# Optimization experiments

Hardware: AMD Instinct MI355X
Metric: run time of the kernel (lower is better)

Reference implementation:

```python
import jax, jax.numpy as jnp
import numpy as np

B, F, C, W_, H_ = 4, 8, 256, 7, 7   # batch, frames, compressed channels (in_dim//r), width, height
CIN = 2048                          # in_dim
CH = CIN // 16                      # in_dim // (2*r) = 128, per-branch q/k channels


def _pw2d(x, W, b):
    # 1x1 Conv2d == per-pixel channel matmul. x: (N,Cin,H,W), W: (Cout,Cin)
    return jnp.einsum('nchw,oc->nohw', x, W) + b[None, :, None, None]


def setup_inputs() -> dict:
    key = jax.random.key(0)
    ks = iter(jax.random.split(key, 40))
    def rn(shape, s=0.02):
        return jax.random.normal(next(ks), shape, dtype=jnp.float32) * s
    inp = {
        'x':       rn((B * F, CIN, H_, W_), 1.0),
        'domainX': rn((B * F, CIN, H_, W_), 1.0),
        'domainY': rn((B * F, 1, H_, W_), 1.0),
        # conv1_1_pre (1 -> 2048), output is discarded in forward but computed faithfully
        'w_pre': rn((CIN, 1)), 'b_pre': rn((CIN,)),
        # conv3 (2048 -> 256); its weight is SHARED with layer1_downconv and layer1_downconv_Y
        'w_conv3': rn((C, CIN)), 'b_conv3': rn((C,)),
        # value_conv 1x1x1 Conv3d (256 -> 2048); weight SHARED with layer1_upconv(_Y)
        'w_value': rn((CIN, C)), 'b_value': rn((CIN,)),
        # tied-weight convs have their own biases
        'b_l1down': rn((C,)), 'b_l1up': rn((CIN,)),
        'b_l1down_Y': rn((C,)), 'b_l1up_Y': rn((CIN,)),
        # layer2 convs: independent weights (layer2_*gamma init to 0, so init add is a no-op)
        'w_l2down': rn((C, CIN)), 'b_l2down': rn((C,)),
        'w_l2up': rn((CIN, C)), 'b_l2up': rn((CIN,)),
        'w_l2down_Y': rn((C, CIN)), 'b_l2down_Y': rn((C,)),
        'w_l2up_Y': rn((CIN, C)), 'b_l2up_Y': rn((CIN,)),
        # q/k projections (2048 -> 128 each)
        'w_c11': rn((CH, CIN)), 'b_c11': rn((CH,)),
        'w_c12': rn((CH, CIN)), 'b_c12': rn((CH,)),
        'w_c21': rn((CH, CIN)), 'b_c21': rn((CH,)),
        'w_c22': rn((CH, CIN)), 'b_c22': rn((CH,)),
        'pos_embedV': rn((1, F, C * H_ * W_), 1.0),
        'gamma': jnp.asarray(0.01, dtype=jnp.float32),
    }
    return inp


def reference(x, domainX, domainY, w_pre, b_pre, w_conv3, b_conv3, w_value, b_value,
              b_l1down, b_l1up, b_l1down_Y, b_l1up_Y,
              w_l2down, b_l2down, w_l2up, b_l2up,
              w_l2down_Y, b_l2down_Y, w_l2up_Y, b_l2up_Y,
              w_c11, b_c11, w_c12, b_c12, w_c21, b_c21, w_c22, b_c22,
              pos_embedV, gamma):
    S = F * W_ * H_  # 392 tokens per clip
    # conv1_1_pre output is overwritten in the original forward (dead computation)
    _dead = _pw2d(domainY, w_pre, b_pre)
    del _dead
    # domainY path: down(conv3 weight) -> up(value_conv weight) -> layer2 down -> layer2 up
    # (create5D/create4D + permutes + 1x1x1 conv3d collapse to pointwise channel matmuls)
    dY = _pw2d(_pw2d(_pw2d(_pw2d(domainX, w_conv3, b_l1down_Y), w_value, b_l1up_Y),
                     w_l2down_Y, b_l2down_Y), w_l2up_Y, b_l2up_Y)
    q4 = jnp.concatenate([_pw2d(x, w_c11, b_c11), _pw2d(dY, w_c12, b_c12)], axis=1)  # (32,256,7,7)
    q = q4.reshape(B, F, C, W_, H_).transpose(0, 1, 3, 4, 2).reshape(B, S, C)
    # domainX path (same structure, shared layer1 weights, its own biases)
    dX = _pw2d(_pw2d(_pw2d(_pw2d(domainX, w_conv3, b_l1down), w_value, b_l1up),
                     w_l2down, b_l2down), w_l2up, b_l2up)
    k4 = jnp.concatenate([_pw2d(x, w_c21, b_c21), _pw2d(dX, w_c22, b_c22)], axis=1)
    k5 = k4.reshape(B, F, C, W_, H_).transpose(0, 1, 3, 4, 2)        # (B,F,W,H,C)
    k = k5.transpose(0, 2, 1, 3, 4).reshape(B, C, S)                 # faithful odd permute
    # value: conv3 -> +pos_embed -> rearrange to (B, S, C)
    v4 = _pw2d(x, w_conv3, b_conv3)                                  # (32,256,7,7)
    v = v4.reshape(B, F, C * W_ * H_) + pos_embedV                   # dropout p=0 is identity
    v = v.reshape(B, F, C, W_, H_).transpose(0, 1, 3, 4, 2).reshape(B, S, C)
    attn = jax.nn.softmax(jnp.einsum('bnc,bcm->bnm', q, k), axis=-1)  # (B,392,392)
    out = jnp.einsum('bnm,bmc->bnc', attn, v)
    out = out.reshape(B, F, W_, H_, C).transpose(0, 4, 1, 2, 3)      # (B,C,F,W,H)
    out = jnp.einsum('bcthw,oc->bothw', out, w_value) + b_value[None, :, None, None, None]
    out = out.transpose(0, 2, 1, 3, 4).reshape(B * F, CIN, W_, H_)
    return (gamma * out + x) * out + x
```

## Files before the change

kernel.cpp:

```cpp
#include <hip/hip_runtime.h>
#include <hip/hip_bf16.h>


typedef __attribute__((ext_vector_type(8))) _Float16 half8;
typedef __attribute__((ext_vector_type(4))) float f32x4;

#define TOKENS 1568

__device__ __forceinline__ ushort f2h(float f) {
    _Float16 h = (_Float16)f;
    return *(ushort*)&h;
}
__device__ __forceinline__ float h2f(ushort u) {
    _Float16 h = *(_Float16*)&u;
    return (float)h;
}

__device__ __forceinline__ void gl16(const void* g, void* l) {
    __builtin_amdgcn_global_load_lds(
        (const __attribute__((address_space(1))) unsigned int*)g,
        (__attribute__((address_space(3))) unsigned int*)l, 16, 0, 0);
}

#define EPI_PART  0
#define EPI_F16   1
#define EPI_FINAL 2

struct GA {
    const ushort* Ah; int lda; long sA;
    const ushort* Wh; int ldw; long sW;
    const float* bias; int sB;
    int nkc, Kc;
    float* fO; ushort* bO;
    int ldc; long sC; int M, N;
    int nx, ny;
    const float *ex, *gamma; float* fout;
};

template<int EPI>
__device__ __forceinline__ void gmm_body(const GA g, int bx, int by, int bzf,
                                         ushort* LA, ushort* LW)
{
    const int tid = threadIdx.x;
    const int bz = bzf / g.nkc;
    const int kc = bzf % g.nkc;
    const int row0 = by * 64, col0 = bx * 128;

    const int srow = tid >> 2;
    const int sq   = (tid & 3) ^ (srow & 3);
    int am  = row0 + srow;      if (am  > g.M - 1) am  = g.M - 1;
    int wn0 = col0 + srow;      if (wn0 > g.N - 1) wn0 = g.N - 1;
    int wn1 = col0 + 64 + srow; if (wn1 > g.N - 1) wn1 = g.N - 1;
    const long kbase = (long)kc * g.Kc + sq * 8;
    const ushort* gA  = g.Ah + bz * g.sA + (long)am  * g.lda + kbase;
    const ushort* gW0 = g.Wh + bz * g.sW + (long)wn0 * g.ldw + kbase;
    const ushort* gW1 = g.Wh + bz * g.sW + (long)wn1 * g.ldw + kbase;
    const int wb = (tid & 192) * 8;

    auto STAGE = [&](int buf, int k0) {
        gl16(gA + k0, LA + buf * 2048 + wb);
        gl16(gW0 + k0, LW + buf * 4096 + wb);
        gl16(gW1 + k0, LW + buf * 4096 + 2048 + wb);
    };

    const int lane = tid & 63, wv = tid >> 6;
    const int wr = (wv >> 1) * 32, wc = (wv & 1) * 64;
    const int fr = lane & 15;
    const int ksw = ((lane >> 4) ^ (lane & 3)) * 8;
    int aoff[2], boff[4];
#pragma unroll
    for (int mi = 0; mi < 2; ++mi) aoff[mi] = (wr + mi * 16 + fr) * 32 + ksw;
#pragma unroll
    for (int ni = 0; ni < 4; ++ni) boff[ni] = (wc + ni * 16 + fr) * 32 + ksw;

    f32x4 acc[2][4];
#pragma unroll
    for (int mi = 0; mi < 2; ++mi)
#pragma unroll
        for (int ni = 0; ni < 4; ++ni) acc[mi][ni] = (f32x4){0.f, 0.f, 0.f, 0.f};

    STAGE(0, 0);
    __syncthreads();
    int cur = 0;
    for (int k0 = 0; k0 < g.Kc; k0 += 32) {
        if (k0 + 32 < g.Kc) STAGE(cur ^ 1, k0 + 32);

        half8 fa[2], fb[4];
#pragma unroll
        for (int mi = 0; mi < 2; ++mi) fa[mi] = *(half8*)&LA[cur * 2048 + aoff[mi]];
#pragma unroll
        for (int ni = 0; ni < 4; ++ni) fb[ni] = *(half8*)&LW[cur * 4096 + boff[ni]];
#pragma unroll
        for (int mi = 0; mi < 2; ++mi)
#pragma unroll
            for (int ni = 0; ni < 4; ++ni)
                acc[mi][ni] = __builtin_amdgcn_mfma_f32_16x16x32_f16(fa[mi], fb[ni], acc[mi][ni], 0, 0, 0);
        __syncthreads();
        cur ^= 1;
    }

    const int q4 = (lane >> 4) * 4;
    float gg = 0.f;
    if constexpr (EPI == EPI_FINAL) gg = g.gamma[0];
#pragma unroll
    for (int mi = 0; mi < 2; ++mi)
#pragma unroll
        for (int ni = 0; ni < 4; ++ni)
#pragma unroll
            for (int qi = 0; qi < 4; ++qi) {
                int m = row0 + wr + mi * 16 + q4 + qi;
                int n = col0 + wc + ni * 16 + fr;
                if (m >= g.M || n >= g.N) continue;
                float v = acc[mi][ni][qi];
                if (g.bias) v += g.bias[bz * g.sB + n];
                if constexpr (EPI == EPI_PART) {
                    g.fO[(long)bzf * g.sC + (long)m * g.ldc + n] = v;
                } else if constexpr (EPI == EPI_F16) {
                    g.bO[(long)bzf * g.sC + (long)m * g.ldc + n] = f2h(v);
                } else {
                    int nimg = m / 49, p = m % 49;
                    long xi = (long)nimg * (2048 * 49) + (long)n * 49 + p;
                    float xv = g.ex[xi];
                    g.fout[xi] = (gg * v + xv) * v + xv;
                }
            }
}

template<int EPI>
__global__ __launch_bounds__(256)
void gmm(GA g)
{
    __shared__ __align__(16) ushort LA[2 * 2048], LW[2 * 4096];
    gmm_body<EPI>(g, blockIdx.x, blockIdx.y, blockIdx.z, LA, LW);
}

__global__ __launch_bounds__(256)
void gmm3(GA g1, int n1, GA g2, int n2, GA g3)
{
    __shared__ __align__(16) ushort LA[2 * 2048], LW[2 * 4096];
    int id = blockIdx.x;
    if (id < n1) {
        int bx = id % g1.nx, t = id / g1.nx;
        gmm_body<EPI_PART>(g1, bx, t % g1.ny, t / g1.ny, LA, LW);
    } else if (id < n1 + n2) {
        id -= n1;
        int bx = id % g2.nx, t = id / g2.nx;
        gmm_body<EPI_PART>(g2, bx, t % g2.ny, t / g2.ny, LA, LW);
    } else {
        id -= n1 + n2;
        int bx = id % g3.nx, t = id / g3.nx;
        gmm_body<EPI_PART>(g3, bx, t % g3.ny, t / g3.ny, LA, LW);
    }
}

__global__ __launch_bounds__(256)
void prep(const float* c11, const float* c21, const float* conv3,
          const float* c22, const float* c12, const float* wval,
          const float* w2dX, const float* w2dY,
          const float* b_c11, const float* b_c21, const float* b_conv3,
          const float* x, const float* dX,
          const float* w2u, const float* w2uY, const float* wv, const float* w3,
          ushort* Wg1, ushort* C2, ushort* Wval, ushort* W2dS, float* bg1,
          ushort* Xt, ushort* DXt,
          ushort* W2uT, ushort* WvT, ushort* W3T)
{
    __shared__ float tile[64][65];
    int b = blockIdx.x;
    int tid = threadIdx.x;
    if (b < 12290) {
        int e = b * 256 + tid;
        if (e < 1048576) {
            float v = e < 262144 ? c11[e] : e < 524288 ? c21[e - 262144] : conv3[e - 524288];
            Wg1[e] = f2h(v);
        } else if (e < 1572864) {
            int i = e - 1048576;
            C2[i] = f2h(i < 262144 ? c22[i] : c12[i - 262144]);
        } else if (e < 2097152) {
            int i = e - 1572864; Wval[i] = f2h(wval[i]);
        } else if (e < 2097664) {
            int i = e - 2097152;
            bg1[i] = i < 128 ? b_c11[i] : i < 256 ? b_c21[i - 128] : b_conv3[i - 256];
        } else {
            int i = e - 2097664;
            W2dS[i] = f2h(i < 524288 ? w2dX[i] : w2dY[i - 524288]);
        }
    } else if (b < 14338) {
        int local = b - 12290;
        int z = local >> 10;
        int rem = local & 1023;
        int n = rem & 31, c0 = (rem >> 5) * 64;
        const float* src = z ? dX : x;
        ushort* oh = z ? DXt : Xt;
        const float* s = src + (long)n * (2048 * 49) + (long)c0 * 49;
        for (int idx = tid; idx < 64 * 49; idx += 256)
            tile[idx / 49][idx % 49] = s[idx];
        __syncthreads();
        for (int idx = tid; idx < 49 * 64; idx += 256) {
            int p = idx >> 6, cl = idx & 63;
            long o = (long)(n * 49 + p) * 2048 + c0 + cl;
            oh[o] = f2h(tile[cl][p]);
        }
    } else {
        int local = b - 14338;
        int zc = local >> 7, t = local & 127;
        const float* src; ushort* dh; int rows;
        switch (zc) {
            case 0:  src = w2u;  dh = W2uT;          rows = 2048; break;
            case 1:  src = w2uY; dh = W2uT + 524288; rows = 2048; break;
            case 2:  src = wv;   dh = WvT;           rows = 2048; break;
            default: src = w3;   dh = W3T;           rows = 256;  break;
        }
        int cols = 524288 / rows;
        int tilesX = cols >> 6;
        int tx = t % tilesX, ty = t / tilesX;
        for (int i = tid; i < 4096; i += 256) {
            int r = i >> 6, c = i & 63;
            tile[r][c] = src[(long)(ty * 64 + r) * cols + tx * 64 + c];
        }
        __syncthreads();
        for (int i = tid; i < 4096; i += 256) {
            int c = i >> 6, r = i & 63;
            long o = (long)(tx * 64 + c) * rows + ty * 64 + r;
            dh[o] = f2h(tile[r][c]);
        }
    }
}

__global__ __launch_bounds__(256)
void redA(const float* __restrict__ PG1, const float* __restrict__ bg1,
          const float* __restrict__ pos,
          ushort* Q, ushort* Km, ushort* V,
          const float* __restrict__ A1p, ushort* A1,
          const float* __restrict__ Dp, ushort* DT,
          const float* w2dX, const float* w2dY,
          const float* b1dX, const float* b1uX, const float* b2dX,
          const float* b1dY, const float* b1uY, const float* b2dY,
          float* __restrict__ dvec)
{
    int blk = blockIdx.x, tid = threadIdx.x;
    if (blk < 3136) {
        int idx = blk * 256 + tid;
        int m = idx >> 9, n = idx & 511;
        float v = bg1[n];
#pragma unroll
        for (int k = 0; k < 8; ++k) v += PG1[(long)k * 802816 + idx];
        int p = m % 49, img = m / 49;
        int f = img & 7, b = img >> 3;
        if (n < 128) {
            Q[m * 256 + n] = f2h(v);
        } else if (n < 256) {
            int c = n - 128;
            int flat = (p / 7) * 14336 + f * 1792 + (p % 7) * 256 + c;
            int ci = flat / 392, mm = flat % 392;
            Km[(long)b * 100352 + (long)mm * 256 + ci] = f2h(v);
        } else {
            int c = n - 256;
            v += pos[f * 12544 + c * 49 + p];
            int s = m % 392;
            long o = (long)b * 106496 + (long)c * 416 + s;
            V[o] = f2h(v);
            if (s < 24) V[o + 392] = 0;
        }
    } else if (blk < 3200) {
        int b2 = blk - 3136;
#pragma unroll
        for (int r = 0; r < 4; ++r) {
            int idx = b2 * 1024 + r * 256 + tid;
            int z = idx >> 15, e = idx & 32767;
            float v = 0.f;
#pragma unroll
            for (int k = 0; k < 8; ++k) v += A1p[(long)(z * 8 + k) * 32768 + e];
            A1[idx] = f2h(v);
        }
    } else if (blk < 3232) {
        int b2 = blk - 3200;
#pragma unroll
        for (int r = 0; r < 16; ++r) {
            int idx = b2 * 4096 + r * 256 + tid;
            int z = idx >> 16, e = idx & 65535;
            int i = e >> 8, j = e & 255;
            float v = 0.f;
#pragma unroll
            for (int k = 0; k < 8; ++k) v += Dp[(long)(z * 8 + k) * 65536 + e];
            DT[(long)z * 65536 + (long)j * 256 + i] = f2h(v);
        }
    } else {
        int blk2 = blk - 3232;
        int z = blk2 >> 6;
        int lane = tid & 63, wv = tid >> 6;
        int c = (blk2 & 63) * 4 + wv;
        const float* w2d = (z ? w2dY : w2dX) + (long)c * 2048;
        const float* b1d = z ? b1dY : b1dX;
        const float* b1u = z ? b1uY : b1uX;
        const float* b2d = z ? b2dY : b2dX;
        float acc = 0.f;
        for (int o = lane; o < 2048; o += 64) acc = fmaf(w2d[o], b1u[o], acc);
        for (int j = lane; j < 256; j += 64) {
            float d = 0.f;
#pragma unroll
            for (int k = 0; k < 8; ++k) d += Dp[(long)(z * 8 + k) * 65536 + (long)c * 256 + j];
            acc = fmaf(d, b1d[j], acc);
        }
        for (int off = 32; off; off >>= 1) acc += __shfl_down(acc, off, 64);
        if (lane == 0) dvec[z * 256 + c] = acc + b2d[c];
    }
}

__global__ __launch_bounds__(256)
void mkc(GA gM,
         const ushort* __restrict__ A1, const float* __restrict__ dvec,
         const float* c22, const float* c12,
         const float* b2uX, const float* b2uY,
         const float* bc22, const float* bc12, float* kc)
{
    __shared__ __align__(16) ushort LA[2 * 2048], LW[2 * 4096];
    int id = blockIdx.x;
    if (id < 64) {
        gmm_body<EPI_F16>(gM, id & 15, (id >> 4) & 1, id >> 5, LA, LW);
        return;
    }
    int tid = threadIdx.x, lane = tid & 63, wv = tid >> 6;
    int w = (id - 64) * 4 + wv;
    int z = w >> 7, i = w & 127;
    const ushort* a1 = A1 + (long)z * 32768 + i * 256;
    const float* dv = dvec + z * 256;
    const float* cr = (z ? c12 : c22) + (long)i * 2048;
    const float* b2u = z ? b2uY : b2uX;
    float acc = 0.f;
    for (int c = lane; c < 256; c += 64) acc = fmaf(h2f(a1[c]), dv[c], acc);
    for (int o = lane; o < 2048; o += 64) acc = fmaf(cr[o], b2u[o], acc);
    for (int off = 32; off; off >>= 1) acc += __shfl_down(acc, off, 64);
    if (lane == 0) kc[z * 128 + i] = acc + (z ? bc12 : bc22)[i];
}

__global__ __launch_bounds__(256)
void r_qk2(const float* __restrict__ P, const float* __restrict__ kc,
           ushort* Q, ushort* Km)
{
    int idx = blockIdx.x * 256 + threadIdx.x;
    int m = idx >> 8, j = idx & 255;
    float v = kc[j];
#pragma unroll
    for (int k = 0; k < 8; ++k) v += P[(long)k * 401408 + idx];
    ushort h = f2h(v);
    if (j < 128) {
        int c = 128 + j;
        int p = m % 49, img = m / 49, f = img & 7, b = img >> 3;
        int flat = (p / 7) * 14336 + f * 1792 + (p % 7) * 256 + c;
        int ci = flat / 392, mm = flat % 392;
        Km[(long)b * 100352 + (long)mm * 256 + ci] = h;
    } else {
        Q[m * 256 + j] = h;
    }
}

__global__ __launch_bounds__(256)
void fattn(const ushort* __restrict__ Qg, const ushort* __restrict__ Kmg,
           const ushort* __restrict__ VT, ushort* __restrict__ O)
{
    __shared__ float raw[16 * 420];
    __shared__ ushort P[16 * 424];
    const int b = blockIdx.y;
    const int r0 = blockIdx.x * 16;
    const int tid = threadIdx.x;
    const int lane = tid & 63, wv = tid >> 6;
    const int fr = lane & 15, g = lane >> 4;
    const int kb = g * 8;
    const long base = (long)b * 100352;
    const long vbase = (long)b * 106496;

    int qr = r0 + fr; if (qr > 391) qr = 391;
    const ushort* qp = Qg + base + (long)qr * 256 + kb;
    half8 qh[8];
#pragma unroll
    for (int kf = 0; kf < 8; ++kf) qh[kf] = *(const half8*)(qp + kf * 32);

    for (int nf = wv; nf < 26; nf += 4) {
        int kcol = nf * 16 + fr; if (kcol > 391) kcol = 391;
        const ushort* kp = Kmg + base + (long)kcol * 256 + kb;
        f32x4 a = (f32x4){0.f, 0.f, 0.f, 0.f};
#pragma unroll
        for (int kf = 0; kf < 8; ++kf) {
            half8 bh = *(const half8*)(kp + kf * 32);
            a = __builtin_amdgcn_mfma_f32_16x16x32_f16(qh[kf], bh, a, 0, 0, 0);
        }
#pragma unroll
        for (int q = 0; q < 4; ++q)
            raw[(g * 4 + q) * 420 + nf * 16 + fr] = a[q];
    }
    __syncthreads();

    {
        int row = tid >> 4, j = tid & 15;
        float v[26];
        float m = -1e30f;
#pragma unroll
        for (int k = 0; k < 26; ++k) {
            int col = j + 16 * k;
            v[k] = (col < 392) ? raw[row * 420 + col] : -1e30f;
            m = fmaxf(m, v[k]);
        }
#pragma unroll
        for (int off = 8; off; off >>= 1) m = fmaxf(m, __shfl_xor(m, off, 16));
        float s = 0.f;
#pragma unroll
        for (int k = 0; k < 26; ++k) { v[k] = __expf(v[k] - m); s += v[k]; }
#pragma unroll
        for (int off = 8; off; off >>= 1) s += __shfl_xor(s, off, 16);
        float inv = 1.f / s;
#pragma unroll
        for (int k = 0; k < 26; ++k) {
            int col = j + 16 * k;
            P[row * 424 + col] = (col < 392) ? f2h(v[k] * inv) : (ushort)0;
        }
    }
    __syncthreads();

    const int cf0 = wv * 4;
    f32x4 o[4];
#pragma unroll
    for (int c = 0; c < 4; ++c) o[c] = (f32x4){0.f, 0.f, 0.f, 0.f};
#pragma unroll
    for (int kf = 0; kf < 13; ++kf) {
        half8 pa = *(half8*)&P[fr * 424 + kf * 32 + kb];
#pragma unroll
        for (int c = 0; c < 4; ++c) {
            const ushort* vp = VT + vbase + (long)((cf0 + c) * 16 + fr) * 416 + kf * 32 + kb;
            half8 vb = *(const half8*)vp;
            o[c] = __builtin_amdgcn_mfma_f32_16x16x32_f16(pa, vb, o[c], 0, 0, 0);
        }
    }
#pragma unroll
    for (int c = 0; c < 4; ++c)
#pragma unroll
        for (int q = 0; q < 4; ++q) {
            int orow = r0 + g * 4 + q;
            if (orow < 392)
                O[base + (long)orow * 256 + (cf0 + c) * 16 + fr] = f2h(o[c][q]);
        }
}

extern "C" void kernel_launch(void* const* d_in, const int* in_sizes, int n_in,
                              void* d_out, int out_size, void* d_ws, size_t ws_size,
                              hipStream_t stream)
{
    const float* x        = (const float*)d_in[0];
    const float* domainX  = (const float*)d_in[1];
    const float* w_conv3  = (const float*)d_in[5];
    const float* b_conv3  = (const float*)d_in[6];
    const float* w_value  = (const float*)d_in[7];
    const float* b_value  = (const float*)d_in[8];
    const float* b_l1down   = (const float*)d_in[9];
    const float* b_l1up     = (const float*)d_in[10];
    const float* b_l1down_Y = (const float*)d_in[11];
    const float* b_l1up_Y   = (const float*)d_in[12];
    const float* w_l2down   = (const float*)d_in[13];
    const float* b_l2down   = (const float*)d_in[14];
    const float* w_l2up     = (const float*)d_in[15];
    const float* b_l2up     = (const float*)d_in[16];
    const float* w_l2down_Y = (const float*)d_in[17];
    const float* b_l2down_Y = (const float*)d_in[18];
    const float* w_l2up_Y   = (const float*)d_in[19];
    const float* b_l2up_Y   = (const float*)d_in[20];
    const float* w_c11 = (const float*)d_in[21];
    const float* b_c11 = (const float*)d_in[22];
    const float* w_c12 = (const float*)d_in[23];
    const float* b_c12 = (const float*)d_in[24];
    const float* w_c21 = (const float*)d_in[25];
    const float* b_c21 = (const float*)d_in[26];
    const float* w_c22 = (const float*)d_in[27];
    const float* b_c22 = (const float*)d_in[28];
    const float* pos   = (const float*)d_in[29];
    const float* gamma = (const float*)d_in[30];
    float* out = (float*)d_out;

    ushort* U = (ushort*)d_ws;
    float*  Fp = (float*)d_ws;

    const long oXt   = 0;
    const long oDXt  = 3211264;
    const long oWg1  = 6422528;
    const long oWval = 7471104;
    const long oC2   = 7995392;
    const long oW2uT = 8519680;
    const long oWvT  = 9568256;
    const long oW3T  = 10092544;
    const long oW2dS = 10616832;
    const long oQ    = 11665408;
    const long oKm   = 12066816;
    const long oVT   = 12468224;
    const long oA1   = 12894208;
    const long oDT   = 12959744;
    const long oA3   = 13090816;
    const long oM    = 13156352;
    const long oO    = 13680640;
    const long fPG1  = 7041024;
    const long fA1p  = 13463552;
    const long fDp   = 13987840;
    const long fPG2  = 15036416;
    const long fbg1  = 18247680;
    const long fkc   = 18248192;
    const long fdv   = 18248448;

    GA Z = {};

    prep<<<dim3(14850), 256, 0, stream>>>(
        w_c11, w_c21, w_conv3, w_c22, w_c12, w_value, w_l2down, w_l2down_Y,
        b_c11, b_c21, b_conv3, x, domainX,
        w_l2up, w_l2up_Y, w_value, w_conv3,
        U + oWg1, U + oC2, U + oWval, U + oW2dS, Fp + fbg1,
        U + oXt, U + oDXt,
        U + oW2uT, U + oWvT, U + oW3T);

    {
        GA g1 = Z;
        g1.Ah = U + oXt; g1.lda = 2048; g1.sA = 0;
        g1.Wh = U + oWg1; g1.ldw = 2048; g1.sW = 0;
        g1.nkc = 8; g1.Kc = 256; g1.fO = Fp + fPG1;
        g1.ldc = 512; g1.sC = 802816; g1.M = TOKENS; g1.N = 512; g1.nx = 4; g1.ny = 25;
        GA ga1 = Z;
        ga1.Ah = U + oC2; ga1.lda = 2048; ga1.sA = 262144;
        ga1.Wh = U + oW2uT; ga1.ldw = 2048; ga1.sW = 524288;
        ga1.nkc = 8; ga1.Kc = 256; ga1.fO = Fp + fA1p;
        ga1.ldc = 256; ga1.sC = 32768; ga1.M = 128; ga1.N = 256; ga1.nx = 2; ga1.ny = 2;
        GA gd = Z;
        gd.Ah = U + oW2dS; gd.lda = 2048; gd.sA = 524288;
        gd.Wh = U + oWvT; gd.ldw = 2048; gd.sW = 0;
        gd.nkc = 8; gd.Kc = 256; gd.fO = Fp + fDp;
        gd.ldc = 256; gd.sC = 65536; gd.M = 256; gd.N = 256; gd.nx = 2; gd.ny = 4;
        gmm3<<<dim3(992), 256, 0, stream>>>(g1, 800, ga1, 64, gd);
    }

    redA<<<dim3(3360), 256, 0, stream>>>(Fp + fPG1, Fp + fbg1, pos,
        U + oQ, U + oKm, U + oVT,
        Fp + fA1p, U + oA1,
        Fp + fDp, U + oDT,
        w_l2down, w_l2down_Y,
        b_l1down, b_l1up, b_l2down,
        b_l1down_Y, b_l1up_Y, b_l2down_Y,
        Fp + fdv);

    {
        GA g = Z;
        g.Ah = U + oA1; g.lda = 256; g.sA = 32768;
        g.Wh = U + oDT; g.ldw = 256; g.sW = 65536;
        g.nkc = 1; g.Kc = 256; g.bO = U + oA3;
        g.ldc = 256; g.sC = 32768; g.M = 128; g.N = 256; g.nx = 2; g.ny = 2;
        gmm<EPI_F16><<<dim3(2, 2, 2), 256, 0, stream>>>(g);
    }

    {
        GA g = Z;
        g.Ah = U + oA3; g.lda = 256; g.sA = 32768;
        g.Wh = U + oW3T; g.ldw = 256; g.sW = 0;
        g.nkc = 1; g.Kc = 256; g.bO = U + oM;
        g.ldc = 2048; g.sC = 262144; g.M = 128; g.N = 2048; g.nx = 16; g.ny = 2;
        mkc<<<dim3(128), 256, 0, stream>>>(g,
            U + oA1, Fp + fdv,
            w_c22, w_c12, b_l2up, b_l2up_Y,
            b_c22, b_c12, Fp + fkc);
    }

    {
        GA g = Z;
        g.Ah = U + oDXt; g.lda = 2048; g.sA = 0;
        g.Wh = U + oM; g.ldw = 2048; g.sW = 0;
        g.nkc = 8; g.Kc = 256; g.fO = Fp + fPG2;
        g.ldc = 256; g.sC = 401408; g.M = TOKENS; g.N = 256; g.nx = 2; g.ny = 25;
        gmm<EPI_PART><<<dim3(2, 25, 8), 256, 0, stream>>>(g);
    }

    r_qk2<<<dim3(1568), 256, 0, stream>>>(Fp + fPG2, Fp + fkc, U + oQ, U + oKm);

    fattn<<<dim3(25, 4), 256, 0, stream>>>(U + oQ, U + oKm, U + oVT, U + oO);

    {
        GA g = Z;
        g.Ah = U + oO; g.lda = 256; g.sA = 0;
        g.Wh = U + oWval; g.ldw = 256; g.sW = 0;
        g.bias = b_value; g.sB = 0;
        g.nkc = 1; g.Kc = 256;
        g.ldc = 0; g.sC = 0; g.M = TOKENS; g.N = 2048; g.nx = 16; g.ny = 25;
        g.ex = x; g.gamma = gamma; g.fout = out;
        gmm<EPI_FINAL><<<dim3(16, 25, 1), 256, 0, stream>>>(g);
    }
}
```

Measured before the change: 149.3 us.

## Reassociate dX q/k chain: project domainX by conv3 first, then small GEMM

Changes the matrix chain for the domainX q/k projection. Instead of building M = A3·W3 (2048-wide) and multiplying the token matrix by it with K=2048, it computes P0 = domainX·W_conv3ᵀ (N=256) inside the first fused GEMM launch and then runs a small K=256 GEMM against A3. That GEMM's epilogue writes Q and the permuted K directly, which removes the mkc M-build, the split-K partial buffer and the separate r_qk2 reduction kernel. The cost is a larger first GEMM launch and extra reduction work in redA, plus a different rounding order because P0 is stored in fp16.

Result: no change. 147.8 us (-1.0%).

```diff
diff --git a/kernel.cpp b/kernel.cpp
--- a/kernel.cpp
+++ b/kernel.cpp
@@ -24,14 +24,15 @@
 
 #define EPI_PART  0
 #define EPI_F16   1
-#define EPI_FINAL 2
+#define EPI_QK2   2
+#define EPI_FINAL 3
 
 struct GA {
     const ushort* Ah; int lda; long sA;
     const ushort* Wh; int ldw; long sW;
     const float* bias; int sB;
     int nkc, Kc;
-    float* fO; ushort* bO;
+    float* fO; ushort* bO; ushort* bO2;
     int ldc; long sC; int M, N;
     int nx, ny;
     const float *ex, *gamma; float* fout;
@@ -117,6 +118,17 @@
                     g.fO[(long)bzf * g.sC + (long)m * g.ldc + n] = v;
                 } else if constexpr (EPI == EPI_F16) {
                     g.bO[(long)bzf * g.sC + (long)m * g.ldc + n] = f2h(v);
+                } else if constexpr (EPI == EPI_QK2) {
+                    ushort h = f2h(v);
+                    if (n < 128) {
+                        int c = 128 + n;
+                        int p = m % 49, img = m / 49, f = img & 7, b = img >> 3;
+                        int flat = (p / 7) * 14336 + f * 1792 + (p % 7) * 256 + c;
+                        int ci = flat / 392, mm = flat % 392;
+                        g.bO2[(long)b * 100352 + (long)mm * 256 + ci] = h;
+                    } else {
+                        g.bO[m * 256 + n] = h;
+                    }
                 } else {
                     int nimg = m / 49, p = m % 49;
                     long xi = (long)nimg * (2048 * 49) + (long)n * 49 + p;
@@ -135,7 +147,7 @@
 }
 
 __global__ __launch_bounds__(256)
-void gmm3(GA g1, int n1, GA g2, int n2, GA g3)
+void gmm4(GA g1, int n1, GA g2, int n2, GA g3, int n3, GA g4)
 {
     __shared__ __align__(16) ushort LA[2 * 2048], LW[2 * 4096];
     int id = blockIdx.x;
@@ -146,10 +158,14 @@
         id -= n1;
         int bx = id % g2.nx, t = id / g2.nx;
         gmm_body<EPI_PART>(g2, bx, t % g2.ny, t / g2.ny, LA, LW);
-    } else {
+    } else if (id < n1 + n2 + n3) {
         id -= n1 + n2;
         int bx = id % g3.nx, t = id / g3.nx;
         gmm_body<EPI_PART>(g3, bx, t % g3.ny, t / g3.ny, LA, LW);
+    } else {
+        id -= n1 + n2 + n3;
+        int bx = id % g4.nx, t = id / g4.nx;
+        gmm_body<EPI_PART>(g4, bx, t % g4.ny, t / g4.ny, LA, LW);
     }
 }
 
@@ -159,10 +175,10 @@
           const float* w2dX, const float* w2dY,
           const float* b_c11, const float* b_c21, const float* b_conv3,
           const float* x, const float* dX,
-          const float* w2u, const float* w2uY, const float* wv, const float* w3,
+          const float* w2u, const float* w2uY, const float* wv,
           ushort* Wg1, ushort* C2, ushort* Wval, ushort* W2dS, float* bg1,
           ushort* Xt, ushort* DXt,
-          ushort* W2uT, ushort* WvT, ushort* W3T)
+          ushort* W2uT, ushort* WvT)
 {
     __shared__ float tile[64][65];
     int b = blockIdx.x;
@@ -203,14 +219,13 @@
     } else {
         int local = b - 14338;
         int zc = local >> 7, t = local & 127;
-        const float* src; ushort* dh; int rows;
+        const float* src; ushort* dh;
         switch (zc) {
-            case 0:  src = w2u;  dh = W2uT;          rows = 2048; break;
-            case 1:  src = w2uY; dh = W2uT + 524288; rows = 2048; break;
-            case 2:  src = wv;   dh = WvT;           rows = 2048; break;
-            default: src = w3;   dh = W3T;           rows = 256;  break;
-        }
-        int cols = 524288 / rows;
+            case 0:  src = w2u;  dh = W2uT;          break;
+            case 1:  src = w2uY; dh = W2uT + 524288; break;
+            default: src = wv;   dh = WvT;           break;
+        }
+        const int rows = 2048, cols = 256;
         int tilesX = cols >> 6;
         int tx = t % tilesX, ty = t / tilesX;
         for (int i = tid; i < 4096; i += 256) {
@@ -232,6 +247,7 @@
           ushort* Q, ushort* Km, ushort* V,
           const float* __restrict__ A1p, ushort* A1,
           const float* __restrict__ Dp, ushort* DT,
+          const float* __restrict__ P0p, ushort* P0,
           const float* w2dX, const float* w2dY,
           const float* b1dX, const float* b1uX, const float* b2dX,
           const float* b1dY, const float* b1uY, const float* b2dY,
@@ -284,7 +300,7 @@
             for (int k = 0; k < 8; ++k) v += Dp[(long)(z * 8 + k) * 65536 + e];
             DT[(long)z * 65536 + (long)j * 256 + i] = f2h(v);
         }
-    } else {
+    } else if (blk < 3360) {
         int blk2 = blk - 3232;
         int z = blk2 >> 6;
         int lane = tid & 63, wv = tid >> 6;
@@ -303,24 +319,31 @@
         }
         for (int off = 32; off; off >>= 1) acc += __shfl_down(acc, off, 64);
         if (lane == 0) dvec[z * 256 + c] = acc + b2d[c];
+    } else {
+        int idx = (blk - 3360) * 256 + tid;
+        float v = 0.f;
+#pragma unroll
+        for (int k = 0; k < 4; ++k) v += P0p[(long)k * 401408 + idx];
+        P0[idx] = f2h(v);
     }
 }
 
 __global__ __launch_bounds__(256)
-void mkc(GA gM,
-         const ushort* __restrict__ A1, const float* __restrict__ dvec,
-         const float* c22, const float* c12,
-         const float* b2uX, const float* b2uY,
-         const float* bc22, const float* bc12, float* kc)
+void a3kc(GA gA3,
+          const ushort* __restrict__ A1, const float* __restrict__ dvec,
+          const float* c22, const float* c12,
+          const float* b2uX, const float* b2uY,
+          const float* bc22, const float* bc12, float* kc)
 {
     __shared__ __align__(16) ushort LA[2 * 2048], LW[2 * 4096];
     int id = blockIdx.x;
-    if (id < 64) {
-        gmm_body<EPI_F16>(gM, id & 15, (id >> 4) & 1, id >> 5, LA, LW);
+    if (id < 8) {
+        int bx = id & 1, t = id >> 1;
+        gmm_body<EPI_F16>(gA3, bx, t & 1, t >> 1, LA, LW);
         return;
     }
     int tid = threadIdx.x, lane = tid & 63, wv = tid >> 6;
-    int w = (id - 64) * 4 + wv;
+    int w = (id - 8) * 4 + wv;
     int z = w >> 7, i = w & 127;
     const ushort* a1 = A1 + (long)z * 32768 + i * 256;
     const float* dv = dvec + z * 256;
@@ -331,27 +354,6 @@
     for (int o = lane; o < 2048; o += 64) acc = fmaf(cr[o], b2u[o], acc);
     for (int off = 32; off; off >>= 1) acc += __shfl_down(acc, off, 64);
     if (lane == 0) kc[z * 128 + i] = acc + (z ? bc12 : bc22)[i];
-}
-
-__global__ __launch_bounds__(256)
-void r_qk2(const float* __restrict__ P, const float* __restrict__ kc,
-           ushort* Q, ushort* Km)
-{
-    int idx = blockIdx.x * 256 + threadIdx.x;
-    int m = idx >> 8, j = idx & 255;
-    float v = kc[j];
-#pragma unroll
-    for (int k = 0; k < 8; ++k) v += P[(long)k * 401408 + idx];
-    ushort h = f2h(v);
-    if (j < 128) {
-        int c = 128 + j;
-        int p = m % 49, img = m / 49, f = img & 7, b = img >> 3;
-        int flat = (p / 7) * 14336 + f * 1792 + (p % 7) * 256 + c;
-        int ci = flat / 392, mm = flat % 392;
-        Km[(long)b * 100352 + (long)mm * 256 + ci] = h;
-    } else {
-        Q[m * 256 + j] = h;
-    }
 }
 
 __global__ __launch_bounds__(256)
@@ -484,33 +486,32 @@
     const long oC2   = 7995392;
     const long oW2uT = 8519680;
     const long oWvT  = 9568256;
-    const long oW3T  = 10092544;
-    const long oW2dS = 10616832;
-    const long oQ    = 11665408;
-    const long oKm   = 12066816;
-    const long oVT   = 12468224;
-    const long oA1   = 12894208;
-    const long oDT   = 12959744;
-    const long oA3   = 13090816;
-    const long oM    = 13156352;
-    const long oO    = 13680640;
-    const long fPG1  = 7041024;
-    const long fA1p  = 13463552;
-    const long fDp   = 13987840;
-    const long fPG2  = 15036416;
-    const long fbg1  = 18247680;
-    const long fkc   = 18248192;
-    const long fdv   = 18248448;
+    const long oW2dS = 10092544;
+    const long oQ    = 11141120;
+    const long oKm   = 11542528;
+    const long oVT   = 11943936;
+    const long oA1   = 12369920;
+    const long oDT   = 12435456;
+    const long oA3   = 12566528;
+    const long oP0   = 12632064;
+    const long oO    = 13033472;
+    const long fPG1  = 6979584;
+    const long fP0p  = 13402112;
+    const long fA1p  = 15007744;
+    const long fDp   = 15532032;
+    const long fbg1  = 16580608;
+    const long fkc   = 16581120;
+    const long fdv   = 16581376;
 
     GA Z = {};
 
-    prep<<<dim3(14850), 256, 0, stream>>>(
+    prep<<<dim3(14722), 256, 0, stream>>>(
         w_c11, w_c21, w_conv3, w_c22, w_c12, w_value, w_l2down, w_l2down_Y,
         b_c11, b_c21, b_conv3, x, domainX,
-        w_l2up, w_l2up_Y, w_value, w_conv3,
+        w_l2up, w_l2up_Y, w_value,
         U + oWg1, U + oC2, U + oWval, U + oW2dS, Fp + fbg1,
         U + oXt, U + oDXt,
-        U + oW2uT, U + oWvT, U + oW3T);
+        U + oW2uT, U + oWvT);
 
     {
         GA g1 = Z;
@@ -528,13 +529,19 @@
         gd.Wh = U + oWvT; gd.ldw = 2048; gd.sW = 0;
         gd.nkc = 8; gd.Kc = 256; gd.fO = Fp + fDp;
         gd.ldc = 256; gd.sC = 65536; gd.M = 256; gd.N = 256; gd.nx = 2; gd.ny = 4;
-        gmm3<<<dim3(992), 256, 0, stream>>>(g1, 800, ga1, 64, gd);
-    }
-
-    redA<<<dim3(3360), 256, 0, stream>>>(Fp + fPG1, Fp + fbg1, pos,
+        GA gp = Z;
+        gp.Ah = U + oDXt; gp.lda = 2048; gp.sA = 0;
+        gp.Wh = U + oWg1 + 524288; gp.ldw = 2048; gp.sW = 0;
+        gp.nkc = 4; gp.Kc = 512; gp.fO = Fp + fP0p;
+        gp.ldc = 256; gp.sC = 401408; gp.M = TOKENS; gp.N = 256; gp.nx = 2; gp.ny = 25;
+        gmm4<<<dim3(1192), 256, 0, stream>>>(g1, 800, ga1, 64, gd, 128, gp);
+    }
+
+    redA<<<dim3(4928), 256, 0, stream>>>(Fp + fPG1, Fp + fbg1, pos,
         U + oQ, U + oKm, U + oVT,
         Fp + fA1p, U + oA1,
         Fp + fDp, U + oDT,
+        Fp + fP0p, U + oP0,
         w_l2down, w_l2down_Y,
         b_l1down, b_l1up, b_l2down,
         b_l1down_Y, b_l1up_Y, b_l2down_Y,
@@ -546,16 +553,7 @@
         g.Wh = U + oDT; g.ldw = 256; g.sW = 65536;
         g.nkc = 1; g.Kc = 256; g.bO = U + oA3;
         g.ldc = 256; g.sC = 32768; g.M = 128; g.N = 256; g.nx = 2; g.ny = 2;
-        gmm<EPI_F16><<<dim3(2, 2, 2), 256, 0, stream>>>(g);
-    }
-
-    {
-        GA g = Z;
-        g.Ah = U + oA3; g.lda = 256; g.sA = 32768;
-        g.Wh = U + oW3T; g.ldw = 256; g.sW = 0;
-        g.nkc = 1; g.Kc = 256; g.bO = U + oM;
-        g.ldc = 2048; g.sC = 262144; g.M = 128; g.N = 2048; g.nx = 16; g.ny = 2;
-        mkc<<<dim3(128), 256, 0, stream>>>(g,
+        a3kc<<<dim3(72), 256, 0, stream>>>(g,
             U + oA1, Fp + fdv,
             w_c22, w_c12, b_l2up, b_l2up_Y,
             b_c22, b_c12, Fp + fkc);
@@ -563,14 +561,14 @@
 
     {
         GA g = Z;
-        g.Ah = U + oDXt; g.lda = 2048; g.sA = 0;
-        g.Wh = U + oM; g.ldw = 2048; g.sW = 0;
-        g.nkc = 8; g.Kc = 256; g.fO = Fp + fPG2;
-        g.ldc = 256; g.sC = 401408; g.M = TOKENS; g.N = 256; g.nx = 2; g.ny = 25;
-        gmm<EPI_PART><<<dim3(2, 25, 8), 256, 0, stream>>>(g);
-    }
-
-    r_qk2<<<dim3(1568), 256, 0, stream>>>(Fp + fPG2, Fp + fkc, U + oQ, U + oKm);
+        g.Ah = U + oP0; g.lda = 256; g.sA = 0;
+        g.Wh = U + oA3; g.ldw = 256; g.sW = 0;
+        g.bias = Fp + fkc; g.sB = 0;
+        g.nkc = 1; g.Kc = 256;
+        g.bO = U + oQ; g.bO2 = U + oKm;
+        g.ldc = 0; g.sC = 0; g.M = TOKENS; g.N = 256; g.nx = 2; g.ny = 25;
+        gmm<EPI_QK2><<<dim3(2, 25, 1), 256, 0, stream>>>(g);
+    }
 
     fattn<<<dim3(25, 4), 256, 0, stream>>>(U + oQ, U + oKm, U + oVT, U + oO);
 
```
